# Kernel tuning notes

Hardware: AMD Instinct MI355X
Metric: run time of the kernel (lower is better)

The kernel has to match this reference:

```python
import jax, jax.numpy as jnp
import numpy as np

B, K = 16, 50
IN_CH, N_CLASSES, N_ANCH = 256, 80, 3
STRIDE, FSIZE, IGNORE_THRE = 8, 76, 0.7
N_CH = 5 + N_CLASSES
ANCHORS = np.array([[10,13],[16,30],[33,23],[30,61],[62,45],[59,119],[116,90],[156,198],[373,326]], np.float32)
ALL_GRID = ANCHORS / STRIDE            # all 9 anchors in grid units
ANCH_MASK = np.array([0, 1, 2])        # layer_no = 2
MASKED = ALL_GRID[ANCH_MASK]           # (3,2) anchors used by this head


def setup_inputs():
    key = jax.random.key(0)
    k1, k2, k3, k4, k5, k6 = jax.random.split(key, 6)
    xin = jax.random.normal(k1, (B, IN_CH, FSIZE, FSIZE), jnp.float32)
    cls = jax.random.randint(k2, (B, K), 0, N_CLASSES).astype(jnp.float32)
    xy = jax.random.uniform(k3, (B, K, 2), minval=0.05, maxval=0.95)
    wh = jax.random.uniform(k4, (B, K, 2), minval=0.02, maxval=0.30)
    labels = jnp.concatenate([cls[..., None], xy, wh], -1)   # (B,K,5) [cls,xc,yc,w,h]
    oc = N_ANCH * N_CH
    conv_w = jax.random.normal(k5, (oc, IN_CH), jnp.float32) * 0.01
    conv_b = jax.random.normal(k6, (oc,), jnp.float32) * 0.01
    return {"xin": xin, "labels": labels, "conv_w": conv_w, "conv_b": conv_b}


def _yolo(xin, conv_w, conv_b, labels):
    f, C = FSIZE, N_CLASSES
    # 1x1 conv == channel matmul
    raw = jnp.einsum('bchw,oc->bohw', xin, conv_w) + conv_b[None, :, None, None]
    raw = raw.reshape(B, N_ANCH, N_CH, f, f).transpose(0, 1, 3, 4, 2)  # (B,A,f,f,85)
    # sigmoid on x,y,obj,cls; w,h stay raw
    out = jnp.concatenate([jax.nn.sigmoid(raw[..., :2]), raw[..., 2:4], jax.nn.sigmoid(raw[..., 4:])], -1)

    grid = jnp.arange(f, dtype=jnp.float32)
    mw = jnp.asarray(MASKED[:, 0]); mh = jnp.asarray(MASKED[:, 1])
    px = out[..., 0] + grid[None, None, None, :]
    py = out[..., 1] + grid[None, None, :, None]
    pw = jnp.exp(out[..., 2]) * mw[None, :, None, None]
    ph = jnp.exp(out[..., 3]) * mh[None, :, None, None]
    pred = jax.lax.stop_gradient(jnp.stack([px, py, pw, ph], -1))  # detached, like torch .data

    labels = jax.lax.stop_gradient(labels)
    valid = labels.sum(-1) > 0                  # (B,K) padding rows are all-zero
    tx = labels[..., 1] * f; ty = labels[..., 2] * f
    tw = labels[..., 3] * f; th = labels[..., 4] * f
    ii = tx.astype(jnp.int32); jj = ty.astype(jnp.int32)

    # anchor matching: IoU of [0,0,w,h] truth vs [0,0,aw,ah] ref anchors (corners at origin)
    aw = jnp.asarray(ALL_GRID[:, 0]); ah = jnp.asarray(ALL_GRID[:, 1])
    inter_a = jnp.minimum(tw[..., None], aw) * jnp.minimum(th[..., None], ah)  # (B,K,9)
    iou_a = inter_a / (tw[..., None] * th[..., None] + aw * ah - inter_a)
    best_n_all = jnp.argmax(iou_a, -1)
    best_n = best_n_all % 3
    best_mask = (best_n_all == ANCH_MASK[0]) | (best_n_all == ANCH_MASK[1]) | (best_n_all == ANCH_MASK[2])

    # pred-vs-truth IoU in cxcywh form (xyxy=False)
    pa = pred.reshape(B, -1, 4)                 # (B, A*f*f, 4)
    tb = jnp.stack([tx, ty, tw, th], -1)        # (B, K, 4)
    tl = jnp.maximum(pa[:, :, None, :2] - pa[:, :, None, 2:] * 0.5, tb[:, None, :, :2] - tb[:, None, :, 2:] * 0.5)
    br = jnp.minimum(pa[:, :, None, :2] + pa[:, :, None, 2:] * 0.5, tb[:, None, :, :2] + tb[:, None, :, 2:] * 0.5)
    en = jnp.all(tl < br, -1)
    inter = jnp.prod(br - tl, -1) * en
    area_p = pa[..., 2] * pa[..., 3]; area_t = tb[..., 2] * tb[..., 3]
    iou_p = inter / (area_p[:, :, None] + area_t[:, None, :] - inter)
    iou_p = jnp.where(valid[:, None, :], iou_p, 0.0)
    ignore = (iou_p.max(-1) > IGNORE_THRE).reshape(B, N_ANCH, f, f)
    obj_mask = 1.0 - ignore.astype(jnp.float32)

    # scatter positive targets; non-selected rows routed out-of-bounds and dropped
    sel = valid & best_mask
    bb = jnp.where(sel, jnp.arange(B)[:, None], B)
    obj_mask = obj_mask.at[bb, best_n, jj, ii].set(1.0, mode='drop')
    tgt_mask = jnp.zeros((B, N_ANCH, f, f, 4 + C)).at[bb, best_n, jj, ii].set(1.0, mode='drop')
    scale = jnp.sqrt(2.0 - tw * th / (f * f))
    tgt_scale = jnp.zeros((B, N_ANCH, f, f, 2)).at[bb, best_n, jj, ii].set(
        jnp.broadcast_to(scale[..., None], (B, K, 2)), mode='drop')
    tvals = jnp.concatenate([
        (tx - ii)[..., None], (ty - jj)[..., None],
        jnp.log(tw / mw[best_n] + 1e-16)[..., None],
        jnp.log(th / mh[best_n] + 1e-16)[..., None],
        jnp.ones((B, K, 1), jnp.float32),
        jax.nn.one_hot(labels[..., 0].astype(jnp.int32), C)], -1)  # (B,K,85)
    target = jnp.zeros((B, N_ANCH, f, f, N_CH)).at[bb, best_n, jj, ii].set(tvals, mode='drop')

    oxy = out[..., :2] * tgt_mask[..., :2]
    owh = out[..., 2:4] * tgt_mask[..., 2:4] * tgt_scale
    oob = out[..., 4] * obj_mask
    ocl = out[..., 5:] * tgt_mask[..., 4:]
    txy = target[..., :2] * tgt_mask[..., :2]
    twh = target[..., 2:4] * tgt_mask[..., 2:4] * tgt_scale
    tob = target[..., 4] * obj_mask
    tcl = target[..., 5:] * tgt_mask[..., 4:]

    def bce(p, t, w=None):
        pc = jnp.clip(p, 1e-12, 1.0 - 1e-7)
        e = -(t * jnp.log(pc) + (1.0 - t) * jnp.log(1.0 - pc))
        if w is not None:
            e = e * w
        return e.sum()

    loss_xy = bce(oxy, txy, tgt_scale * tgt_scale)
    loss_wh = 0.5 * jnp.sum((owh - twh) ** 2)
    loss_obj = bce(oob, tob)
    loss_cls = bce(ocl, tcl)
    out_m = jnp.concatenate([oxy, owh, oob[..., None], ocl], -1)
    tgt_m = jnp.concatenate([txy, twh, tob[..., None], tcl], -1)
    loss_l2 = jnp.sum((out_m - tgt_m) ** 2)
    loss = loss_xy + loss_wh + loss_obj + loss_cls
    return loss, loss_xy, loss_wh, loss_obj, loss_cls, loss_l2, out_m


def reference(xin, labels, conv_w, conv_b):
    return _yolo(xin, conv_w, conv_b, labels)
```

## Files before the change

### kernel.cpp

```cpp
#include <hip/hip_runtime.h>
#include <hip/hip_bf16.h>

#define B_   16
#define K_   50
#define CIN  256
#define F_   76
#define A_   3
#define NCH  85
#define OC   255
#define HW   (F_*F_)
#define NBLK (B_*F_)
#define RAWS 84

#define WS_BIAS_F 32768
#define WS_LAB_F  33024
#define WS_PART_F 45824

typedef __attribute__((ext_vector_type(8))) short short8;
typedef __attribute__((ext_vector_type(4))) float f32x4;

__device__ __constant__ float AW9[9] = {1.25f, 2.0f, 4.125f, 3.75f, 7.75f, 7.375f, 14.5f, 19.5f, 46.625f};
__device__ __constant__ float AH9[9] = {1.625f, 3.75f, 2.875f, 7.625f, 5.625f, 14.875f, 11.25f, 24.75f, 40.75f};

__device__ __forceinline__ unsigned short f2bf(float f) {
    union { float f; unsigned int u; } v; v.f = f;
    unsigned int r = v.u + 0x7fffu + ((v.u >> 16) & 1u);
    return (unsigned short)(r >> 16);
}
__device__ __forceinline__ float bf2f(unsigned short b) {
    union { unsigned int u; float f; } v; v.u = ((unsigned int)b) << 16;
    return v.f;
}
__device__ __forceinline__ float sigm(float r) { return 1.0f / (1.0f + __expf(-r)); }
__device__ __forceinline__ float bce_t(float p, float tv) {
    float pc = fminf(fmaxf(p, 1e-12f), 1.0f - 1e-7f);
    return -(tv * __logf(pc) + (1.0f - tv) * __logf(1.0f - pc));
}

__global__ void prep_kernel(const float* __restrict__ conv_w, const float* __restrict__ conv_b,
                            const float* __restrict__ labels, float* __restrict__ ws) {
    int bid = blockIdx.x, t = threadIdx.x;
    if (bid < 256) {
        int idx = bid * 256 + t;
        int mt = idx >> 12, ks = (idx >> 9) & 7, lane = (idx >> 3) & 63, jj = idx & 7;
        int row = mt * 16 + (lane & 15);
        int k   = ks * 32 + (lane >> 4) * 8 + jj;
        float v = (row < OC) ? conv_w[row * CIN + k] : 0.0f;
        ((unsigned short*)ws)[idx] = f2bf(v);
    } else if (bid == 256) {
        ws[WS_BIAS_F + t] = (t < OC) ? conv_b[t] : 0.0f;
    } else {
        for (int idx = t; idx < B_ * K_; idx += 256) {
            const float* L = labels + idx * 5;
            float cls = L[0], xc = L[1], yc = L[2], wl = L[3], hl = L[4];
            float ssum = cls + xc + yc + wl + hl;
            float validf = (ssum > 0.0f) ? 1.0f : 0.0f;
            float tx = xc * F_, ty = yc * F_, tw = wl * F_, th = hl * F_;
            int ii = (int)tx, jj = (int)ty;
            float tarea = tw * th;
            float best = -1.0f; int bn = 0;
            #pragma unroll
            for (int n = 0; n < 9; n++) {
                float inter = fminf(tw, AW9[n]) * fminf(th, AH9[n]);
                float iou = inter / (tarea + AW9[n] * AH9[n] - inter);
                if (iou > best) { best = iou; bn = n; }
            }
            int a = bn % 3;
            bool self = (validf != 0.0f) && (bn < 3);
            float* R = ws + WS_LAB_F + idx * 16;
            R[0] = tx; R[1] = ty; R[2] = tw; R[3] = th;
            R[4] = validf; R[5] = self ? (float)a : -1.0f; R[6] = (float)ii; R[7] = (float)jj;
            R[8] = tx - (float)ii; R[9] = ty - (float)jj;
            R[10] = __logf(tw / AW9[a] + 1e-16f);
            R[11] = __logf(th / AH9[a] + 1e-16f);
            R[12] = sqrtf(2.0f - tarea / (float)HW);
            R[13] = cls; R[14] = 0.0f; R[15] = 0.0f;
        }
    }
}

__global__ __launch_bounds__(256, 3) void yolo_main(const float* __restrict__ xin,
                                                    const float* __restrict__ ws,
                                                    float* __restrict__ d_out,
                                                    float* __restrict__ part) {
    __shared__ __align__(16) unsigned short UNI[OC * RAWS];
    __shared__ float4 LAB[K_ * 4];
    __shared__ float biasS[256];
    __shared__ int   flagS[240];
    __shared__ float omvS[240];
    __shared__ float redS[4][5];

    const int t = threadIdx.x;
    const int b = blockIdx.x / F_;
    const int j = blockIdx.x % F_;

    biasS[t] = ws[WS_BIAS_F + t];
    {
        const float4* wsrec = (const float4*)(ws + WS_LAB_F + b * (K_ * 16));
        if (t < K_ * 4) LAB[t] = wsrec[t];
    }

    for (int idx = t; idx < 32 * F_; idx += 256) {
        int co = idx / F_, i = idx - co * F_;
        const float* xp = xin + ((size_t)b * CIN + co * 8) * HW + j * F_ + i;
        short8 v;
        #pragma unroll
        for (int jj = 0; jj < 8; jj++) v[jj] = (short)f2bf(xp[jj * HW]);
        int phys = co ^ (i & 7);
        *(short8*)&UNI[i * 256 + phys * 8] = v;
    }
    __syncthreads();

    const int w = t >> 6, lane = t & 63, lr = lane & 15, q = lane >> 4;
    f32x4 acc[4][5];
    #pragma unroll
    for (int m = 0; m < 4; m++)
        #pragma unroll
        for (int n = 0; n < 5; n++) acc[m][n] = (f32x4){0.0f, 0.0f, 0.0f, 0.0f};

    const short8* wf = (const short8*)ws;
    #pragma unroll 2
    for (int ks = 0; ks < 8; ks++) {
        short8 afr[4], bfr[5];
        #pragma unroll
        for (int m = 0; m < 4; m++)
            afr[m] = wf[((w * 4 + m) * 8 + ks) * 64 + lane];
        #pragma unroll
        for (int n = 0; n < 5; n++) {
            int nn = n * 16 + lr;
            int phys = (ks * 4 + q) ^ (nn & 7);
            bfr[n] = *(const short8*)&UNI[nn * 256 + phys * 8];
        }
        #pragma unroll
        for (int m = 0; m < 4; m++)
            #pragma unroll
            for (int n = 0; n < 5; n++)
                acc[m][n] = __builtin_amdgcn_mfma_f32_16x16x32_bf16(afr[m], bfr[n], acc[m][n], 0, 0, 0);
    }
    __syncthreads();

    #pragma unroll
    for (int m = 0; m < 4; m++) {
        #pragma unroll
        for (int n = 0; n < 5; n++) {
            int i = n * 16 + lr;
            if (i < F_) {
                #pragma unroll
                for (int r = 0; r < 4; r++) {
                    int o = (w * 4 + m) * 16 + q * 4 + r;
                    if (o < OC) UNI[o * RAWS + i] = f2bf(acc[m][n][r] + biasS[o]);
                }
            }
        }
    }
    __syncthreads();

    float lxy = 0.0f, lwh = 0.0f, lobj = 0.0f, lcls = 0.0f, l2 = 0.0f;
    if (t < A_ * F_) {
        int a = t / F_, i = t - a * F_;
        const unsigned short* rc = UNI + (a * NCH) * RAWS + i;
        float x   = sigm(bf2f(rc[0 * RAWS]));
        float y   = sigm(bf2f(rc[1 * RAWS]));
        float wr  = bf2f(rc[2 * RAWS]);
        float hr  = bf2f(rc[3 * RAWS]);
        float obj = sigm(bf2f(rc[4 * RAWS]));

        float px = x + (float)i, py = y + (float)j;
        float pw = __expf(wr) * AW9[a], ph = __expf(hr) * AH9[a];
        float hpw = pw * 0.5f, hph = ph * 0.5f;
        float areap = pw * ph;
        float fa_t = (float)a, fi_t = (float)i, fj_t = (float)j;

        float maxiou = 0.0f; int mk = -1;
        #pragma unroll 2
        for (int k = 0; k < K_; k++) {
            float4 A0 = LAB[4 * k + 0];
            float4 A1 = LAB[4 * k + 1];
            float tx = A0.x, ty = A0.y, tw = A0.z, th = A0.w;
            float tlx = fmaxf(px - hpw, tx - tw * 0.5f);
            float tly = fmaxf(py - hph, ty - th * 0.5f);
            float brx = fminf(px + hpw, tx + tw * 0.5f);
            float bry = fminf(py + hph, ty + th * 0.5f);
            float iw = brx - tlx, ih = bry - tly;
            float inter = (iw > 0.0f && ih > 0.0f) ? iw * ih : 0.0f;
            float iou = __fdividef(inter, areap + tw * th - inter);
            iou = (A1.x != 0.0f) ? iou : 0.0f;
            maxiou = fmaxf(maxiou, iou);
            bool match = (A1.y == fa_t) & (A1.z == fi_t) & (A1.w == fj_t);
            mk = match ? k : mk;
        }
        float objmask = (maxiou > 0.7f) ? 0.0f : 1.0f;

        if (mk >= 0) {
            float4 B0 = LAB[4 * mk + 2];
            float4 B1 = LAB[4 * mk + 3];
            float sc = B0.x;
            sc = B1.x;
            float sc2 = sc * sc;
            float txv = B0.x, tyv = B0.y, twv = B0.z, thv = B0.w;
            int cl = (int)B1.y;
            lxy = (bce_t(x, txv) + bce_t(y, tyv)) * sc2;
            float dw = wr - twv, dh = hr - thv;
            lwh = 0.5f * sc2 * (dw * dw + dh * dh);
            float pco = fminf(fmaxf(obj, 1e-12f), 1.0f - 1e-7f);
            lobj = -__logf(pco);
            float dx = x - txv, dy = y - tyv, dob = obj - 1.0f;
            l2 = dx * dx + dy * dy + sc2 * (dw * dw + dh * dh) + dob * dob;
            for (int c = 0; c < 80; c++) {
                float p = sigm(bf2f(rc[(5 + c) * RAWS]));
                float tcv = (c == cl) ? 1.0f : 0.0f;
                lcls += bce_t(p, tcv);
                float d = p - tcv;
                l2 += d * d;
            }
            flagS[t] = mk + 1;
            omvS[t]  = obj;
        } else {
            float oo = obj * objmask;
            if (objmask != 0.0f) {
                float pco = fminf(obj, 1.0f - 1e-7f);
                lobj = -__logf(1.0f - pco);
            }
            l2 = oo * oo;
            flagS[t] = 0;
            omvS[t]  = oo;
        }
    }
    __syncthreads();

    for (int a = 0; a < A_; a++) {
        float* dst = d_out + 6 + ((((size_t)(b * A_ + a)) * F_ + j) * F_) * NCH;
        for (int idx = t; idx < F_ * NCH; idx += 256) {
            int i  = idx / NCH;
            int ch = idx - i * NCH;
            int cell = a * F_ + i;
            int flag = flagS[cell];
            float v;
            if (flag == 0) {
                v = (ch == 4) ? omvS[cell] : 0.0f;
            } else {
                float raw = bf2f(UNI[(a * NCH + ch) * RAWS + i]);
                if (ch == 2 || ch == 3) v = raw * LAB[4 * (flag - 1) + 3].x;
                else                    v = sigm(raw);
            }
            dst[idx] = v;
        }
    }

    #pragma unroll
    for (int off = 32; off > 0; off >>= 1) {
        lxy  += __shfl_down(lxy, off);
        lwh  += __shfl_down(lwh, off);
        lobj += __shfl_down(lobj, off);
        lcls += __shfl_down(lcls, off);
        l2   += __shfl_down(l2, off);
    }
    if (lane == 0) {
        redS[w][0] = lxy; redS[w][1] = lwh; redS[w][2] = lobj;
        redS[w][3] = lcls; redS[w][4] = l2;
    }
    __syncthreads();
    if (t == 0) {
        float* P = part + (size_t)blockIdx.x * 8;
        #pragma unroll
        for (int q2 = 0; q2 < 5; q2++)
            P[q2] = redS[0][q2] + redS[1][q2] + redS[2][q2] + redS[3][q2];
    }
}

__global__ void finish_kernel(const float* __restrict__ part, float* __restrict__ d_out) {
    int t = threadIdx.x;
    float s0 = 0, s1 = 0, s2 = 0, s3 = 0, s4 = 0;
    for (int bidx = t; bidx < NBLK; bidx += 256) {
        const float* P = part + (size_t)bidx * 8;
        s0 += P[0]; s1 += P[1]; s2 += P[2]; s3 += P[3]; s4 += P[4];
    }
    #pragma unroll
    for (int off = 32; off > 0; off >>= 1) {
        s0 += __shfl_down(s0, off); s1 += __shfl_down(s1, off);
        s2 += __shfl_down(s2, off); s3 += __shfl_down(s3, off);
        s4 += __shfl_down(s4, off);
    }
    __shared__ float red[4][5];
    if ((t & 63) == 0) {
        int w = t >> 6;
        red[w][0] = s0; red[w][1] = s1; red[w][2] = s2; red[w][3] = s3; red[w][4] = s4;
    }
    __syncthreads();
    if (t == 0) {
        float r0 = red[0][0] + red[1][0] + red[2][0] + red[3][0];
        float r1 = red[0][1] + red[1][1] + red[2][1] + red[3][1];
        float r2 = red[0][2] + red[1][2] + red[2][2] + red[3][2];
        float r3 = red[0][3] + red[1][3] + red[2][3] + red[3][3];
        float r4 = red[0][4] + red[1][4] + red[2][4] + red[3][4];
        d_out[0] = r0 + r1 + r2 + r3;
        d_out[1] = r0; d_out[2] = r1; d_out[3] = r2; d_out[4] = r3; d_out[5] = r4;
    }
}

extern "C" void kernel_launch(void* const* d_in, const int* in_sizes, int n_in,
                              void* d_out, int out_size, void* d_ws, size_t ws_size,
                              hipStream_t stream) {
    const float* xin    = (const float*)d_in[0];
    const float* labels = (const float*)d_in[1];
    const float* conv_w = (const float*)d_in[2];
    const float* conv_b = (const float*)d_in[3];
    float* out  = (float*)d_out;
    float* ws   = (float*)d_ws;
    float* part = ws + WS_PART_F;

    prep_kernel<<<258, 256, 0, stream>>>(conv_w, conv_b, labels, ws);
    yolo_main<<<NBLK, 256, 0, stream>>>(xin, ws, out, part);
    finish_kernel<<<1, 256, 0, stream>>>(part, out);
}
```

Baseline: 235.9 us.

## Double block size to 512 threads, store raw outputs cell-major, vectorize output writes

```diff
diff --git a/kernel.cpp b/kernel.cpp
--- a/kernel.cpp
+++ b/kernel.cpp
@@ -10,7 +10,7 @@
 #define OC   255
 #define HW   (F_*F_)
 #define NBLK (B_*F_)
-#define RAWS 84
+#define NCELL (A_*F_)
 
 #define WS_BIAS_F 32768
 #define WS_LAB_F  33024
@@ -79,28 +79,25 @@
     }
 }
 
-__global__ __launch_bounds__(256, 3) void yolo_main(const float* __restrict__ xin,
+__global__ __launch_bounds__(512, 4) void yolo_main(const float* __restrict__ xin,
                                                     const float* __restrict__ ws,
                                                     float* __restrict__ d_out,
                                                     float* __restrict__ part) {
-    __shared__ __align__(16) unsigned short UNI[OC * RAWS];
+    __shared__ __align__(16) unsigned short UNI[19456];
     __shared__ float4 LAB[K_ * 4];
     __shared__ float biasS[256];
-    __shared__ int   flagS[240];
-    __shared__ float omvS[240];
-    __shared__ float redS[4][5];
+    __shared__ int   flagS[NCELL];
+    __shared__ float omvS[NCELL];
+    __shared__ float redS[8][5];
 
     const int t = threadIdx.x;
     const int b = blockIdx.x / F_;
     const int j = blockIdx.x % F_;
 
-    biasS[t] = ws[WS_BIAS_F + t];
-    {
-        const float4* wsrec = (const float4*)(ws + WS_LAB_F + b * (K_ * 16));
-        if (t < K_ * 4) LAB[t] = wsrec[t];
-    }
-
-    for (int idx = t; idx < 32 * F_; idx += 256) {
+    if (t < 256) biasS[t] = ws[WS_BIAS_F + t];
+    if (t < K_ * 4) LAB[t] = ((const float4*)(ws + WS_LAB_F + b * (K_ * 16)))[t];
+
+    for (int idx = t; idx < 32 * F_; idx += 512) {
         int co = idx / F_, i = idx - co * F_;
         const float* xp = xin + ((size_t)b * CIN + co * 8) * HW + j * F_ + i;
         short8 v;
@@ -112,19 +109,19 @@
     __syncthreads();
 
     const int w = t >> 6, lane = t & 63, lr = lane & 15, q = lane >> 4;
-    f32x4 acc[4][5];
+    f32x4 acc[2][5];
     #pragma unroll
-    for (int m = 0; m < 4; m++)
+    for (int m = 0; m < 2; m++)
         #pragma unroll
         for (int n = 0; n < 5; n++) acc[m][n] = (f32x4){0.0f, 0.0f, 0.0f, 0.0f};
 
     const short8* wf = (const short8*)ws;
     #pragma unroll 2
     for (int ks = 0; ks < 8; ks++) {
-        short8 afr[4], bfr[5];
-        #pragma unroll
-        for (int m = 0; m < 4; m++)
-            afr[m] = wf[((w * 4 + m) * 8 + ks) * 64 + lane];
+        short8 afr[2], bfr[5];
+        #pragma unroll
+        for (int m = 0; m < 2; m++)
+            afr[m] = wf[((w + m * 8) * 8 + ks) * 64 + lane];
         #pragma unroll
         for (int n = 0; n < 5; n++) {
             int nn = n * 16 + lr;
@@ -132,7 +129,7 @@
             bfr[n] = *(const short8*)&UNI[nn * 256 + phys * 8];
         }
         #pragma unroll
-        for (int m = 0; m < 4; m++)
+        for (int m = 0; m < 2; m++)
             #pragma unroll
             for (int n = 0; n < 5; n++)
                 acc[m][n] = __builtin_amdgcn_mfma_f32_16x16x32_bf16(afr[m], bfr[n], acc[m][n], 0, 0, 0);
@@ -140,15 +137,19 @@
     __syncthreads();
 
     #pragma unroll
-    for (int m = 0; m < 4; m++) {
+    for (int m = 0; m < 2; m++) {
         #pragma unroll
         for (int n = 0; n < 5; n++) {
             int i = n * 16 + lr;
             if (i < F_) {
                 #pragma unroll
                 for (int r = 0; r < 4; r++) {
-                    int o = (w * 4 + m) * 16 + q * 4 + r;
-                    if (o < OC) UNI[o * RAWS + i] = f2bf(acc[m][n][r] + biasS[o]);
+                    int o = (w + m * 8) * 16 + q * 4 + r;
+                    if (o < OC) {
+                        int a  = o / NCH;
+                        int ch = o - a * NCH;
+                        UNI[(a * F_ + i) * NCH + ch] = f2bf(acc[m][n][r] + biasS[o]);
+                    }
                 }
             }
         }
@@ -156,14 +157,14 @@
     __syncthreads();
 
     float lxy = 0.0f, lwh = 0.0f, lobj = 0.0f, lcls = 0.0f, l2 = 0.0f;
-    if (t < A_ * F_) {
+    if (t < NCELL) {
         int a = t / F_, i = t - a * F_;
-        const unsigned short* rc = UNI + (a * NCH) * RAWS + i;
-        float x   = sigm(bf2f(rc[0 * RAWS]));
-        float y   = sigm(bf2f(rc[1 * RAWS]));
-        float wr  = bf2f(rc[2 * RAWS]);
-        float hr  = bf2f(rc[3 * RAWS]);
-        float obj = sigm(bf2f(rc[4 * RAWS]));
+        const unsigned short* rc = UNI + t * NCH;
+        float x   = sigm(bf2f(rc[0]));
+        float y   = sigm(bf2f(rc[1]));
+        float wr  = bf2f(rc[2]);
+        float hr  = bf2f(rc[3]);
+        float obj = sigm(bf2f(rc[4]));
 
         float px = x + (float)i, py = y + (float)j;
         float pw = __expf(wr) * AW9[a], ph = __expf(hr) * AH9[a];
@@ -194,9 +195,7 @@
         if (mk >= 0) {
             float4 B0 = LAB[4 * mk + 2];
             float4 B1 = LAB[4 * mk + 3];
-            float sc = B0.x;
-            sc = B1.x;
-            float sc2 = sc * sc;
+            float sc = B1.x, sc2 = sc * sc;
             float txv = B0.x, tyv = B0.y, twv = B0.z, thv = B0.w;
             int cl = (int)B1.y;
             lxy = (bce_t(x, txv) + bce_t(y, tyv)) * sc2;
@@ -207,7 +206,7 @@
             float dx = x - txv, dy = y - tyv, dob = obj - 1.0f;
             l2 = dx * dx + dy * dy + sc2 * (dw * dw + dh * dh) + dob * dob;
             for (int c = 0; c < 80; c++) {
-                float p = sigm(bf2f(rc[(5 + c) * RAWS]));
+                float p = sigm(bf2f(rc[5 + c]));
                 float tcv = (c == cl) ? 1.0f : 0.0f;
                 lcls += bce_t(p, tcv);
                 float d = p - tcv;
@@ -229,21 +228,28 @@
     __syncthreads();
 
     for (int a = 0; a < A_; a++) {
-        float* dst = d_out + 6 + ((((size_t)(b * A_ + a)) * F_ + j) * F_) * NCH;
-        for (int idx = t; idx < F_ * NCH; idx += 256) {
-            int i  = idx / NCH;
-            int ch = idx - i * NCH;
-            int cell = a * F_ + i;
-            int flag = flagS[cell];
-            float v;
-            if (flag == 0) {
-                v = (ch == 4) ? omvS[cell] : 0.0f;
-            } else {
-                float raw = bf2f(UNI[(a * NCH + ch) * RAWS + i]);
-                if (ch == 2 || ch == 3) v = raw * LAB[4 * (flag - 1) + 3].x;
-                else                    v = sigm(raw);
-            }
-            dst[idx] = v;
+        float2* dst = (float2*)(d_out + 6 + (size_t)((b * A_ + a) * F_ + j) * F_ * NCH);
+        for (int idx2 = t; idx2 < (F_ * NCH) / 2; idx2 += 512) {
+            int p = idx2 << 1;
+            int i0 = p / NCH;
+            int c0 = p - i0 * NCH;
+            int i1 = i0, c1 = c0 + 1;
+            if (c1 == NCH) { i1++; c1 = 0; }
+            float v[2];
+            int iv[2] = {i0, i1}, cv[2] = {c0, c1};
+            #pragma unroll
+            for (int e = 0; e < 2; e++) {
+                int cell = a * F_ + iv[e];
+                int flag = flagS[cell];
+                if (flag == 0) {
+                    v[e] = (cv[e] == 4) ? omvS[cell] : 0.0f;
+                } else {
+                    float raw = bf2f(UNI[cell * NCH + cv[e]]);
+                    if (cv[e] == 2 || cv[e] == 3) v[e] = raw * LAB[4 * (flag - 1) + 3].x;
+                    else                          v[e] = sigm(raw);
+                }
+            }
+            dst[idx2] = make_float2(v[0], v[1]);
         }
     }
 
@@ -263,8 +269,12 @@
     if (t == 0) {
         float* P = part + (size_t)blockIdx.x * 8;
         #pragma unroll
-        for (int q2 = 0; q2 < 5; q2++)
-            P[q2] = redS[0][q2] + redS[1][q2] + redS[2][q2] + redS[3][q2];
+        for (int q2 = 0; q2 < 5; q2++) {
+            float s = 0.0f;
+            #pragma unroll
+            for (int ww = 0; ww < 8; ww++) s += redS[ww][q2];
+            P[q2] = s;
+        }
     }
 }
 
@@ -310,6 +320,6 @@
     float* part = ws + WS_PART_F;
 
     prep_kernel<<<258, 256, 0, stream>>>(conv_w, conv_b, labels, ws);
-    yolo_main<<<NBLK, 256, 0, stream>>>(xin, ws, out, part);
+    yolo_main<<<NBLK, 512, 0, stream>>>(xin, ws, out, part);
     finish_kernel<<<1, 256, 0, stream>>>(part, out);
 }
```

Measured after the change: 234.7 us. About the same (-0.5%).
